# Optimization experiments

Measured on AMD Instinct MI355X. Metric: run time of the kernel, lower is better.

Reference implementation:

```python
import jax, jax.numpy as jnp
import numpy as np

B, LX, LY, D = 8, 2048, 2048, 256

def setup_inputs() -> dict:
    key = jax.random.key(0)
    k1, k2, k3, k4 = jax.random.split(key, 4)
    x = jax.random.normal(k1, (B, LX, D), dtype=jnp.float32)
    y = jax.random.normal(k2, (B, LY, D), dtype=jnp.float32)
    y_mask = jax.random.randint(k3, (B, LY), 0, 2).astype(jnp.bool_)
    W = jax.random.normal(k4, (D, D), dtype=jnp.float32) * (1.0 / np.sqrt(D))
    b = jnp.zeros((D,), dtype=jnp.float32)
    return {"x": x, "y": y, "y_mask": y_mask, "W": W, "b": b}

def reference(x, y, y_mask, W, b):
    # shared linear + relu projection (torch Linear: x @ W.T + b)
    x_proj = jax.nn.relu(jnp.einsum('bld,ed->ble', x, W) + b)  # [B,LX,D]
    y_proj = jax.nn.relu(jnp.einsum('bld,ed->ble', y, W) + b)  # [B,LY,D]
    scores = jnp.einsum('bxd,byd->bxy', x_proj, y_proj)        # [B,LX,LY]
    scores = jnp.where(y_mask[:, None, :], -jnp.inf, scores)
    alpha = jax.nn.softmax(scores, axis=-1)                    # [B,LX,LY]
    return jnp.einsum('bxy,byd->bxd', alpha, y)                # [B,LX,D]
```

## Files before the change

### kernel.cpp

```cpp
#include <hip/hip_runtime.h>

typedef __attribute__((ext_vector_type(8))) short short8;
typedef _Float16 half8 __attribute__((ext_vector_type(8)));
typedef __attribute__((ext_vector_type(4))) float f32x4;
typedef __attribute__((ext_vector_type(4))) unsigned int uint4v;
typedef __attribute__((ext_vector_type(2))) unsigned int uint2v;

#define B_   8
#define LX_  2048
#define LY_  2048
#define D_   256
#define NROW (B_ * LX_)

__device__ __forceinline__ unsigned short f2bf(float f) {
  unsigned u = __builtin_bit_cast(unsigned, f);
  u += 0x7FFF + ((u >> 16) & 1);
  return (unsigned short)(u >> 16);
}
__device__ __forceinline__ float bf2f(unsigned short h) {
  unsigned u = ((unsigned)h) << 16;
  return __builtin_bit_cast(float, u);
}

__global__ __launch_bounds__(256) void wsplit_kernel(
    const float* __restrict__ W, unsigned short* __restrict__ Whi,
    unsigned short* __restrict__ Wlo) {
  int i = blockIdx.x * 256 + threadIdx.x;
  float w = W[i];
  unsigned short hi = f2bf(w);
  Whi[i] = hi;
  Wlo[i] = f2bf(w - bf2f(hi));
}

__global__ __launch_bounds__(256) void scan_kernel(
    const int* __restrict__ MASK, int* __restrict__ CIDX,
    int* __restrict__ CPOS, int* __restrict__ Lc) {
  __shared__ int s[256];
  int b = blockIdx.x, t = threadIdx.x;
  int f[8];
  int cnt = 0;
  for (int k = 0; k < 8; ++k) {
    f[k] = (MASK[b * 2048 + t * 8 + k] == 0) ? 1 : 0;
    cnt += f[k];
  }
  s[t] = cnt;
  __syncthreads();
  for (int off = 1; off < 256; off <<= 1) {
    int v = (t >= off) ? s[t - off] : 0;
    __syncthreads();
    s[t] += v;
    __syncthreads();
  }
  if (t == 255) Lc[b] = s[255];
  int off = s[t] - cnt;
  for (int k = 0; k < 8; ++k) {
    int j = t * 8 + k;
    if (f[k]) {
      CIDX[b * 2048 + off] = j;
      CPOS[b * 2048 + j] = b * 2048 + off;
      ++off;
    } else {
      CPOS[b * 2048 + j] = -1;
    }
  }
}

__global__ __launch_bounds__(256) void zero_tail_kernel(
    const int* __restrict__ Lc, _Float16* __restrict__ YPc) {
  int b = blockIdx.x;
  int lc = Lc[b];
  int end = (lc + 31) & ~31;
  int total = (end - lc) * 32;
  for (int c = threadIdx.x; c < total; c += 256) {
    int rr = c >> 5, seg = c & 31;
    uint4v z = {0, 0, 0, 0};
    *(uint4v*)(YPc + (size_t)(b * 2048 + lc + rr) * D_ + seg * 8) = z;
  }
}

__global__ __launch_bounds__(256, 2) void proj_kernel(
    const float* __restrict__ X, const float* __restrict__ Y,
    const float* __restrict__ bias,
    const unsigned short* __restrict__ Whi, const unsigned short* __restrict__ Wlo,
    const int* __restrict__ CPOS,
    _Float16* __restrict__ XP, _Float16* __restrict__ YPc) {
  __shared__ unsigned short Ah[64][40], Al[64][40];
  __shared__ unsigned short Bh[256][40], Bl[256][40];

  int t = threadIdx.x;
  int lane = t & 63, wave = t >> 6;
  int q = lane >> 4, n15 = lane & 15;

  bool isX = blockIdx.x < 256;
  const float* src = isX ? X : Y;
  int m0 = (isX ? blockIdx.x : (blockIdx.x - 256)) * 64;

  f32x4 acc[4][4];
  for (int mt = 0; mt < 4; ++mt)
    for (int nt = 0; nt < 4; ++nt) acc[mt][nt] = (f32x4){0.f, 0.f, 0.f, 0.f};

  int arow = t >> 2, aseg = t & 3;
  int erow = t >> 2, ec = t & 3;

  f32x4 pa[2];
  uint4v pbh[4], pbl[4];
#define PROJ_PF(kc)                                                            \
  {                                                                            \
    for (int i = 0; i < 2; ++i)                                                \
      pa[i] = *(const f32x4*)(src + (size_t)(m0 + arow) * D_ + (kc) * 32 +     \
                              (aseg + i * 4) * 4);                             \
    for (int p = 0; p < 4; ++p) {                                              \
      int e = p * 64 + erow;                                                   \
      pbh[p] = *(const uint4v*)(Whi + (size_t)e * D_ + (kc) * 32 + ec * 8);    \
      pbl[p] = *(const uint4v*)(Wlo + (size_t)e * D_ + (kc) * 32 + ec * 8);    \
    }                                                                          \
  }

  PROJ_PF(0);

  for (int kc = 0; kc < 8; ++kc) {
    __syncthreads();
    for (int i = 0; i < 2; ++i) {
      int seg = aseg + i * 4;
      f32x4 f = pa[i];
      unsigned short h[4], l[4];
      for (int j = 0; j < 4; ++j) {
        h[j] = f2bf(f[j]);
        l[j] = f2bf(f[j] - bf2f(h[j]));
      }
      uint2v vh = {(unsigned)h[0] | ((unsigned)h[1] << 16),
                   (unsigned)h[2] | ((unsigned)h[3] << 16)};
      uint2v vl = {(unsigned)l[0] | ((unsigned)l[1] << 16),
                   (unsigned)l[2] | ((unsigned)l[3] << 16)};
      *(uint2v*)&Ah[arow][seg * 4] = vh;
      *(uint2v*)&Al[arow][seg * 4] = vl;
    }
    for (int p = 0; p < 4; ++p) {
      int e = p * 64 + erow;
      *(uint4v*)&Bh[e][ec * 8] = pbh[p];
      *(uint4v*)&Bl[e][ec * 8] = pbl[p];
    }
    if (kc < 7) PROJ_PF(kc + 1);
    __syncthreads();

    short8 afh[4], afl[4], bfh[4], bfl[4];
    for (int mt = 0; mt < 4; ++mt) {
      afh[mt] = *(const short8*)&Ah[mt * 16 + n15][q * 8];
      afl[mt] = *(const short8*)&Al[mt * 16 + n15][q * 8];
    }
    for (int nt = 0; nt < 4; ++nt) {
      bfh[nt] = *(const short8*)&Bh[wave * 64 + nt * 16 + n15][q * 8];
      bfl[nt] = *(const short8*)&Bl[wave * 64 + nt * 16 + n15][q * 8];
    }
    for (int mt = 0; mt < 4; ++mt)
      for (int nt = 0; nt < 4; ++nt) {
        acc[mt][nt] = __builtin_amdgcn_mfma_f32_16x16x32_bf16(afh[mt], bfh[nt], acc[mt][nt], 0, 0, 0);
        acc[mt][nt] = __builtin_amdgcn_mfma_f32_16x16x32_bf16(afl[mt], bfh[nt], acc[mt][nt], 0, 0, 0);
        acc[mt][nt] = __builtin_amdgcn_mfma_f32_16x16x32_bf16(afh[mt], bfl[nt], acc[mt][nt], 0, 0, 0);
      }
  }
#undef PROJ_PF

  int drow[16];
  for (int mt = 0; mt < 4; ++mt)
    for (int r = 0; r < 4; ++r) {
      int row = m0 + mt * 16 + q * 4 + r;
      drow[mt * 4 + r] = isX ? row : CPOS[row];
    }
  _Float16* dst = isX ? XP : YPc;
  for (int nt = 0; nt < 4; ++nt) {
    int e = wave * 64 + nt * 16 + n15;
    float bv = bias[e];
    for (int mt = 0; mt < 4; ++mt)
      for (int r = 0; r < 4; ++r) {
        int dr = drow[mt * 4 + r];
        if (dr >= 0) {
          float v = acc[mt][nt][r] + bv;
          v = v > 0.f ? v : 0.f;
          dst[(size_t)dr * D_ + e] = (_Float16)v;
        }
      }
  }
}

__global__ __launch_bounds__(256) void gatherT_kernel(
    const float* __restrict__ Y, const int* __restrict__ CIDX,
    const int* __restrict__ Lc, _Float16* __restrict__ YTc) {
  __shared__ _Float16 tile[64][72];
  int id = blockIdx.x;
  int db = id & 3, nb = (id >> 2) & 31, b = id >> 7;
  int lc = Lc[b];
  int end = (lc + 31) & ~31;
  if (nb * 64 >= end) return;
  int t = threadIdx.x;
  int nl = t >> 2, ds = t & 3;
  int j = nb * 64 + nl;
  int idx = (j < lc) ? CIDX[b * 2048 + j] : 0;
  const float* src = Y + (size_t)(b * LY_ + idx) * D_ + db * 64 + ds * 16;
  for (int i = 0; i < 4; ++i) {
    f32x4 f = *(const f32x4*)(src + i * 4);
    for (int k = 0; k < 4; ++k) tile[ds * 16 + i * 4 + k][nl] = (_Float16)f[k];
  }
  __syncthreads();
  int dl = t >> 2, nsub = t & 3;
  uint4v v0 = *(const uint4v*)&tile[dl][nsub * 16];
  uint4v v1 = *(const uint4v*)&tile[dl][nsub * 16 + 8];
  _Float16* dst = YTc + (size_t)(b * D_ + db * 64 + dl) * LY_ + nb * 64 + nsub * 16;
  *(uint4v*)(dst) = v0;
  *(uint4v*)(dst + 8) = v1;
}

__global__ __launch_bounds__(256, 2) void flash_kernel(
    const _Float16* __restrict__ XP, const _Float16* __restrict__ YPc,
    const _Float16* __restrict__ YTc, const int* __restrict__ Lc,
    _Float16* __restrict__ PO, float* __restrict__ Pm, float* __restrict__ Pl) {
  __shared__ _Float16 yp_t[32][264];
  __shared__ _Float16 yT_t[256][40];
  __shared__ _Float16 pbuf[4][16][40];

  int t = threadIdx.x;
  int lane = t & 63, wave = t >> 6;
  int q = lane >> 4, n15 = lane & 15;
  int half = blockIdx.x & 1;
  int xb = (blockIdx.x >> 1) & 31;
  int b = blockIdx.x >> 6;
  int row0 = xb * 64 + wave * 16;

  int lc = Lc[b];
  int T  = (lc + 31) >> 5;
  int T0 = (T + 1) >> 1;
  int tstart = half ? T0 : 0;
  int tend   = half ? T  : T0;

  half8 a[8];
  const _Float16* xrow = XP + (size_t)(b * LX_ + row0 + n15) * D_ + q * 8;
  for (int kk = 0; kk < 8; ++kk) a[kk] = *(const half8*)(xrow + kk * 32);

  half8 lones;
  for (int j = 0; j < 8; ++j) lones[j] = (n15 == 0) ? (_Float16)1 : (_Float16)0;

  float m_r[4];
  for (int r = 0; r < 4; ++r) m_r[r] = -1e30f;
  f32x4 lacc = {0.f, 0.f, 0.f, 0.f};
  f32x4 oacc[16];
  for (int dt = 0; dt < 16; ++dt) oacc[dt] = (f32x4){0.f, 0.f, 0.f, 0.f};

  const _Float16* ypb = YPc + (size_t)b * LY_ * D_;
  const _Float16* yTb = YTc + (size_t)b * D_ * LY_;

  uint4v pr[8];
#define PREFETCH(tt)                                                          \
  {                                                                           \
    int y0p = (tt) * 32;                                                      \
    for (int i = 0; i < 4; ++i) {                                             \
      int c = t + i * 256;                                                    \
      pr[i] = *(const uint4v*)(ypb + (size_t)(y0p + (c >> 5)) * D_ + (c & 31) * 8); \
    }                                                                         \
    for (int i = 0; i < 4; ++i) {                                             \
      int c = t + i * 256;                                                    \
      pr[4 + i] = *(const uint4v*)(yTb + (size_t)(c >> 2) * LY_ + y0p + (c & 3) * 8); \
    }                                                                         \
  }

  if (tstart < tend) PREFETCH(tstart);

  for (int tt = tstart; tt < tend; ++tt) {
    int y0 = tt * 32;
    __syncthreads();
    for (int i = 0; i < 4; ++i) {
      int c = t + i * 256;
      *(uint4v*)&yp_t[c >> 5][(c & 31) * 8] = pr[i];
    }
    for (int i = 0; i < 4; ++i) {
      int c = t + i * 256;
      *(uint4v*)&yT_t[c >> 2][(c & 3) * 8] = pr[4 + i];
    }
    if (tt + 1 < tend) PREFETCH(tt + 1);
    __syncthreads();

    f32x4 S0 = {0.f, 0.f, 0.f, 0.f}, S1 = {0.f, 0.f, 0.f, 0.f};
    for (int kk = 0; kk < 8; ++kk) {
      half8 b0 = *(const half8*)&yp_t[n15][kk * 32 + q * 8];
      S0 = __builtin_amdgcn_mfma_f32_16x16x32_f16(a[kk], b0, S0, 0, 0, 0);
    }
    for (int kk = 0; kk < 8; ++kk) {
      half8 b1 = *(const half8*)&yp_t[16 + n15][kk * 32 + q * 8];
      S1 = __builtin_amdgcn_mfma_f32_16x16x32_f16(a[kk], b1, S1, 0, 0, 0);
    }
    bool mk0 = (y0 + n15) >= lc;
    bool mk1 = (y0 + 16 + n15) >= lc;

    float al[4];
    _Float16 ph0[4], ph1[4];
    bool need = false;
    for (int r = 0; r < 4; ++r) {
      float s0 = mk0 ? -1e30f : S0[r];
      float s1 = mk1 ? -1e30f : S1[r];
      float tm = fmaxf(s0, s1);
      tm = fmaxf(tm, __shfl_xor(tm, 1));
      tm = fmaxf(tm, __shfl_xor(tm, 2));
      tm = fmaxf(tm, __shfl_xor(tm, 4));
      tm = fmaxf(tm, __shfl_xor(tm, 8));
      float mn = fmaxf(m_r[r], tm);
      al[r] = __expf(m_r[r] - mn);
      m_r[r] = mn;
      ph0[r] = (_Float16)__expf(s0 - mn);
      ph1[r] = (_Float16)__expf(s1 - mn);
      need = need || (al[r] != 1.0f);
    }
    if (__ballot(need)) {
      for (int dt = 0; dt < 16; ++dt)
        for (int r = 0; r < 4; ++r) oacc[dt][r] *= al[r];
      for (int r = 0; r < 4; ++r) lacc[r] *= al[r];
    }
    for (int r = 0; r < 4; ++r) {
      pbuf[wave][q * 4 + r][n15] = ph0[r];
      pbuf[wave][q * 4 + r][16 + n15] = ph1[r];
    }
    half8 pa = *(const half8*)&pbuf[wave][n15][q * 8];
    lacc = __builtin_amdgcn_mfma_f32_16x16x32_f16(pa, lones, lacc, 0, 0, 0);
    for (int dt = 0; dt < 16; ++dt) {
      half8 bb = *(const half8*)&yT_t[dt * 16 + n15][q * 8];
      oacc[dt] = __builtin_amdgcn_mfma_f32_16x16x32_f16(pa, bb, oacc[dt], 0, 0, 0);
    }
  }
#undef PREFETCH

  size_t prow = (size_t)(half * B_ + b) * LX_ + row0;
  _Float16* po = PO + prow * D_;
  for (int dt = 0; dt < 16; ++dt)
    for (int r = 0; r < 4; ++r)
      po[(size_t)(q * 4 + r) * D_ + dt * 16 + n15] = (_Float16)oacc[dt][r];
  if (n15 == 0) {
    for (int r = 0; r < 4; ++r) {
      Pm[prow + q * 4 + r] = m_r[r];
      Pl[prow + q * 4 + r] = lacc[r];
    }
  }
}

__global__ __launch_bounds__(256) void merge_kernel(
    const _Float16* __restrict__ PO, const float* __restrict__ Pm,
    const float* __restrict__ Pl, float* __restrict__ OUT) {
  int c = blockIdx.x * 256 + threadIdx.x;
  int row = c >> 5, seg = c & 31;
  float m0 = Pm[row], m1 = Pm[NROW + row];
  float l0 = Pl[row], l1 = Pl[NROW + row];
  float m = fmaxf(m0, m1);
  float w0 = __expf(m0 - m), w1 = __expf(m1 - m);
  float inv = 1.0f / (l0 * w0 + l1 * w1);
  const _Float16* p0 = PO + (size_t)row * D_ + seg * 8;
  const _Float16* p1 = p0 + (size_t)NROW * D_;
  half8 a = *(const half8*)p0;
  half8 bsec = *(const half8*)p1;
  float* o = OUT + (size_t)row * D_ + seg * 8;
  f32x4 o0, o1;
  for (int j = 0; j < 4; ++j) o0[j] = ((float)a[j] * w0 + (float)bsec[j] * w1) * inv;
  for (int j = 0; j < 4; ++j) o1[j] = ((float)a[4 + j] * w0 + (float)bsec[4 + j] * w1) * inv;
  *(f32x4*)o = o0;
  *(f32x4*)(o + 4) = o1;
}

extern "C" void kernel_launch(void* const* d_in, const int* in_sizes, int n_in,
                              void* d_out, int out_size, void* d_ws, size_t ws_size,
                              hipStream_t stream) {
  const float* x     = (const float*)d_in[0];
  const float* y     = (const float*)d_in[1];
  const int*   ymask = (const int*)  d_in[2];
  const float* W     = (const float*)d_in[3];
  const float* bias  = (const float*)d_in[4];
  float* out = (float*)d_out;

  char* ws = (char*)d_ws;
  unsigned short* Whi = (unsigned short*)(ws);
  unsigned short* Wlo = (unsigned short*)(ws + 131072);
  _Float16* XP  = (_Float16*)(ws + 262144);
  _Float16* YPc = (_Float16*)(ws + 262144 + 8388608);
  _Float16* YTc = (_Float16*)(ws + 262144 + 2 * 8388608);
  _Float16* PO  = (_Float16*)(ws + 262144 + 3 * 8388608);
  char* tail = ws + 262144 + 3 * 8388608 + 16777216;
  float* Pm   = (float*)(tail);
  float* Pl   = (float*)(tail + 131072);
  int*   CIDX = (int*)  (tail + 262144);
  int*   CPOS = (int*)  (tail + 262144 + 65536);
  int*   Lc   = (int*)  (tail + 262144 + 131072);

  wsplit_kernel<<<256, 256, 0, stream>>>(W, Whi, Wlo);
  scan_kernel<<<8, 256, 0, stream>>>(ymask, CIDX, CPOS, Lc);
  zero_tail_kernel<<<8, 256, 0, stream>>>(Lc, YPc);
  proj_kernel<<<512, 256, 0, stream>>>(x, y, bias, Whi, Wlo, CPOS, XP, YPc);
  gatherT_kernel<<<1024, 256, 0, stream>>>(y, CIDX, Lc, YTc);
  flash_kernel<<<512, 256, 0, stream>>>(XP, YPc, YTc, Lc, PO, Pm, Pl);
  merge_kernel<<<2048, 256, 0, stream>>>(PO, Pm, Pl, out);
}
```

Before: 166.6 us.

## Pre-split X/Y into bf16 hi/lo planes and merge setup kernels

Adds a separate pass that converts X and Y into bf16 hi/lo planes in the workspace, so the projection GEMM loads ready bf16 tiles instead of converting fp32 in its inner loop. The W split and the mask scan are merged into one launch with vectorized W conversion. The tail-zeroing kernel for the compacted Y projection is removed, and the PO buffer now shares memory with the split planes. The extra pass adds a full read and write of the inputs in exchange for less ALU work inside the GEMM, and dropping the tail zeroing relies on the flash kernel not reading those padding rows.

Result: slower. 172.1 us (+3.3%).

```diff
diff --git a/kernel.cpp b/kernel.cpp
--- a/kernel.cpp
+++ b/kernel.cpp
@@ -11,6 +11,7 @@
 #define LY_  2048
 #define D_   256
 #define NROW (B_ * LX_)
+#define MTOT (2 * NROW)
 
 __device__ __forceinline__ unsigned short f2bf(float f) {
   unsigned u = __builtin_bit_cast(unsigned, f);
@@ -22,21 +23,32 @@
   return __builtin_bit_cast(float, u);
 }
 
-__global__ __launch_bounds__(256) void wsplit_kernel(
+__global__ __launch_bounds__(256) void prep_kernel(
     const float* __restrict__ W, unsigned short* __restrict__ Whi,
-    unsigned short* __restrict__ Wlo) {
-  int i = blockIdx.x * 256 + threadIdx.x;
-  float w = W[i];
-  unsigned short hi = f2bf(w);
-  Whi[i] = hi;
-  Wlo[i] = f2bf(w - bf2f(hi));
-}
-
-__global__ __launch_bounds__(256) void scan_kernel(
+    unsigned short* __restrict__ Wlo,
     const int* __restrict__ MASK, int* __restrict__ CIDX,
     int* __restrict__ CPOS, int* __restrict__ Lc) {
+  int t = threadIdx.x;
+  if (blockIdx.x >= 8) {
+    int base = (blockIdx.x - 8) * 2048 + t * 8;
+    f32x4 f0 = *(const f32x4*)(W + base);
+    f32x4 f1 = *(const f32x4*)(W + base + 4);
+    float v[8] = {f0[0], f0[1], f0[2], f0[3], f1[0], f1[1], f1[2], f1[3]};
+    unsigned short h[8], l[8];
+    for (int j = 0; j < 8; ++j) {
+      h[j] = f2bf(v[j]);
+      l[j] = f2bf(v[j] - bf2f(h[j]));
+    }
+    uint4v vh = {(unsigned)h[0] | ((unsigned)h[1] << 16), (unsigned)h[2] | ((unsigned)h[3] << 16),
+                 (unsigned)h[4] | ((unsigned)h[5] << 16), (unsigned)h[6] | ((unsigned)h[7] << 16)};
+    uint4v vl = {(unsigned)l[0] | ((unsigned)l[1] << 16), (unsigned)l[2] | ((unsigned)l[3] << 16),
+                 (unsigned)l[4] | ((unsigned)l[5] << 16), (unsigned)l[6] | ((unsigned)l[7] << 16)};
+    *(uint4v*)(Whi + base) = vh;
+    *(uint4v*)(Wlo + base) = vl;
+    return;
+  }
   __shared__ int s[256];
-  int b = blockIdx.x, t = threadIdx.x;
+  int b = blockIdx.x;
   int f[8];
   int cnt = 0;
   for (int k = 0; k < 8; ++k) {
@@ -65,21 +77,33 @@
   }
 }
 
-__global__ __launch_bounds__(256) void zero_tail_kernel(
-    const int* __restrict__ Lc, _Float16* __restrict__ YPc) {
-  int b = blockIdx.x;
-  int lc = Lc[b];
-  int end = (lc + 31) & ~31;
-  int total = (end - lc) * 32;
-  for (int c = threadIdx.x; c < total; c += 256) {
-    int rr = c >> 5, seg = c & 31;
-    uint4v z = {0, 0, 0, 0};
-    *(uint4v*)(YPc + (size_t)(b * 2048 + lc + rr) * D_ + seg * 8) = z;
-  }
+__global__ __launch_bounds__(256) void split_xy_kernel(
+    const float* __restrict__ X, const float* __restrict__ Y,
+    unsigned short* __restrict__ XYhi, unsigned short* __restrict__ XYlo) {
+  int bb = blockIdx.x;
+  const float* src;
+  size_t off;
+  if (bb < 2048) { src = X; off = 0; }
+  else           { src = Y; off = (size_t)NROW * D_; bb -= 2048; }
+  size_t e0 = ((size_t)bb * 256 + threadIdx.x) * 8;
+  f32x4 f0 = *(const f32x4*)(src + e0);
+  f32x4 f1 = *(const f32x4*)(src + e0 + 4);
+  float v[8] = {f0[0], f0[1], f0[2], f0[3], f1[0], f1[1], f1[2], f1[3]};
+  unsigned short h[8], l[8];
+  for (int j = 0; j < 8; ++j) {
+    h[j] = f2bf(v[j]);
+    l[j] = f2bf(v[j] - bf2f(h[j]));
+  }
+  uint4v vh = {(unsigned)h[0] | ((unsigned)h[1] << 16), (unsigned)h[2] | ((unsigned)h[3] << 16),
+               (unsigned)h[4] | ((unsigned)h[5] << 16), (unsigned)h[6] | ((unsigned)h[7] << 16)};
+  uint4v vl = {(unsigned)l[0] | ((unsigned)l[1] << 16), (unsigned)l[2] | ((unsigned)l[3] << 16),
+               (unsigned)l[4] | ((unsigned)l[5] << 16), (unsigned)l[6] | ((unsigned)l[7] << 16)};
+  *(uint4v*)(XYhi + off + e0) = vh;
+  *(uint4v*)(XYlo + off + e0) = vl;
 }
 
 __global__ __launch_bounds__(256, 2) void proj_kernel(
-    const float* __restrict__ X, const float* __restrict__ Y,
+    const unsigned short* __restrict__ XYhi, const unsigned short* __restrict__ XYlo,
     const float* __restrict__ bias,
     const unsigned short* __restrict__ Whi, const unsigned short* __restrict__ Wlo,
     const int* __restrict__ CPOS,
@@ -92,8 +116,7 @@
   int q = lane >> 4, n15 = lane & 15;
 
   bool isX = blockIdx.x < 256;
-  const float* src = isX ? X : Y;
-  int m0 = (isX ? blockIdx.x : (blockIdx.x - 256)) * 64;
+  int m0 = blockIdx.x * 64;
 
   f32x4 acc[4][4];
   for (int mt = 0; mt < 4; ++mt)
@@ -102,13 +125,12 @@
   int arow = t >> 2, aseg = t & 3;
   int erow = t >> 2, ec = t & 3;
 
-  f32x4 pa[2];
-  uint4v pbh[4], pbl[4];
+  uint4v pah, pal, pbh[4], pbl[4];
 #define PROJ_PF(kc)                                                            \
   {                                                                            \
-    for (int i = 0; i < 2; ++i)                                                \
-      pa[i] = *(const f32x4*)(src + (size_t)(m0 + arow) * D_ + (kc) * 32 +     \
-                              (aseg + i * 4) * 4);                             \
+    size_t aoff = (size_t)(m0 + arow) * D_ + (kc) * 32 + aseg * 8;             \
+    pah = *(const uint4v*)(XYhi + aoff);                                       \
+    pal = *(const uint4v*)(XYlo + aoff);                                       \
     for (int p = 0; p < 4; ++p) {                                              \
       int e = p * 64 + erow;                                                   \
       pbh[p] = *(const uint4v*)(Whi + (size_t)e * D_ + (kc) * 32 + ec * 8);    \
@@ -120,21 +142,8 @@
 
   for (int kc = 0; kc < 8; ++kc) {
     __syncthreads();
-    for (int i = 0; i < 2; ++i) {
-      int seg = aseg + i * 4;
-      f32x4 f = pa[i];
-      unsigned short h[4], l[4];
-      for (int j = 0; j < 4; ++j) {
-        h[j] = f2bf(f[j]);
-        l[j] = f2bf(f[j] - bf2f(h[j]));
-      }
-      uint2v vh = {(unsigned)h[0] | ((unsigned)h[1] << 16),
-                   (unsigned)h[2] | ((unsigned)h[3] << 16)};
-      uint2v vl = {(unsigned)l[0] | ((unsigned)l[1] << 16),
-                   (unsigned)l[2] | ((unsigned)l[3] << 16)};
-      *(uint2v*)&Ah[arow][seg * 4] = vh;
-      *(uint2v*)&Al[arow][seg * 4] = vl;
-    }
+    *(uint4v*)&Ah[arow][aseg * 8] = pah;
+    *(uint4v*)&Al[arow][aseg * 8] = pal;
     for (int p = 0; p < 4; ++p) {
       int e = p * 64 + erow;
       *(uint4v*)&Bh[e][ec * 8] = pbh[p];
@@ -165,7 +174,7 @@
   for (int mt = 0; mt < 4; ++mt)
     for (int r = 0; r < 4; ++r) {
       int row = m0 + mt * 16 + q * 4 + r;
-      drow[mt * 4 + r] = isX ? row : CPOS[row];
+      drow[mt * 4 + r] = isX ? row : CPOS[row - NROW];
     }
   _Float16* dst = isX ? XP : YPc;
   for (int nt = 0; nt < 4; ++nt) {
@@ -372,23 +381,24 @@
   float* out = (float*)d_out;
 
   char* ws = (char*)d_ws;
-  unsigned short* Whi = (unsigned short*)(ws);
-  unsigned short* Wlo = (unsigned short*)(ws + 131072);
-  _Float16* XP  = (_Float16*)(ws + 262144);
-  _Float16* YPc = (_Float16*)(ws + 262144 + 8388608);
-  _Float16* YTc = (_Float16*)(ws + 262144 + 2 * 8388608);
-  _Float16* PO  = (_Float16*)(ws + 262144 + 3 * 8388608);
-  char* tail = ws + 262144 + 3 * 8388608 + 16777216;
-  float* Pm   = (float*)(tail);
-  float* Pl   = (float*)(tail + 131072);
-  int*   CIDX = (int*)  (tail + 262144);
-  int*   CPOS = (int*)  (tail + 262144 + 65536);
-  int*   Lc   = (int*)  (tail + 262144 + 131072);
-
-  wsplit_kernel<<<256, 256, 0, stream>>>(W, Whi, Wlo);
-  scan_kernel<<<8, 256, 0, stream>>>(ymask, CIDX, CPOS, Lc);
-  zero_tail_kernel<<<8, 256, 0, stream>>>(Lc, YPc);
-  proj_kernel<<<512, 256, 0, stream>>>(x, y, bias, Whi, Wlo, CPOS, XP, YPc);
+  size_t o = 0;
+  unsigned short* Whi  = (unsigned short*)(ws + o); o += 131072;
+  unsigned short* Wlo  = (unsigned short*)(ws + o); o += 131072;
+  unsigned short* XYhi = (unsigned short*)(ws + o);
+  _Float16*       PO   = (_Float16*)(ws + o);       o += (size_t)MTOT * D_ * 2;
+  unsigned short* XYlo = (unsigned short*)(ws + o); o += (size_t)MTOT * D_ * 2;
+  _Float16* XP  = (_Float16*)(ws + o); o += 8388608;
+  _Float16* YPc = (_Float16*)(ws + o); o += 8388608;
+  _Float16* YTc = (_Float16*)(ws + o); o += 8388608;
+  float* Pm   = (float*)(ws + o); o += 131072;
+  float* Pl   = (float*)(ws + o); o += 131072;
+  int*   CIDX = (int*)  (ws + o); o += 65536;
+  int*   CPOS = (int*)  (ws + o); o += 65536;
+  int*   Lc   = (int*)  (ws + o);
+
+  prep_kernel<<<40, 256, 0, stream>>>(W, Whi, Wlo, ymask, CIDX, CPOS, Lc);
+  split_xy_kernel<<<4096, 256, 0, stream>>>(x, y, XYhi, XYlo);
+  proj_kernel<<<512, 256, 0, stream>>>(XYhi, XYlo, bias, Whi, Wlo, CPOS, XP, YPc);
   gatherT_kernel<<<1024, 256, 0, stream>>>(y, CIDX, Lc, YTc);
   flash_kernel<<<512, 256, 0, stream>>>(XP, YPc, YTc, Lc, PO, Pm, Pl);
   merge_kernel<<<2048, 256, 0, stream>>>(PO, Pm, Pl, out);
```

## Split flash attention four ways over keys and fuse prep and projection launches

Applied to the files above, without the earlier changes.

The flash kernel now splits the compacted key range into four parts instead of two, which doubles the grid to 1024 blocks. The merge kernel combines four partial softmax results. The weight split and mask scan are fused into one prep kernel, and the projection and transposed gather are fused into one launch. The zero-tail kernel is removed. This cuts launch count and adds parallelism, but doubles the partial-output traffic written and read by merge, and repeats the per-block query load and output store.

Result: no change. 165.5 us (-0.7%).

```diff
diff --git a/kernel.cpp b/kernel.cpp
--- a/kernel.cpp
+++ b/kernel.cpp
@@ -11,6 +11,7 @@
 #define LY_  2048
 #define D_   256
 #define NROW (B_ * LX_)
+#define NQ   4
 
 __device__ __forceinline__ unsigned short f2bf(float f) {
   unsigned u = __builtin_bit_cast(unsigned, f);
@@ -22,21 +23,32 @@
   return __builtin_bit_cast(float, u);
 }
 
-__global__ __launch_bounds__(256) void wsplit_kernel(
+__global__ __launch_bounds__(256) void prep_kernel(
     const float* __restrict__ W, unsigned short* __restrict__ Whi,
-    unsigned short* __restrict__ Wlo) {
-  int i = blockIdx.x * 256 + threadIdx.x;
-  float w = W[i];
-  unsigned short hi = f2bf(w);
-  Whi[i] = hi;
-  Wlo[i] = f2bf(w - bf2f(hi));
-}
-
-__global__ __launch_bounds__(256) void scan_kernel(
+    unsigned short* __restrict__ Wlo,
     const int* __restrict__ MASK, int* __restrict__ CIDX,
     int* __restrict__ CPOS, int* __restrict__ Lc) {
+  int t = threadIdx.x;
+  if (blockIdx.x >= 8) {
+    int base = (blockIdx.x - 8) * 2048 + t * 8;
+    f32x4 f0 = *(const f32x4*)(W + base);
+    f32x4 f1 = *(const f32x4*)(W + base + 4);
+    float v[8] = {f0[0], f0[1], f0[2], f0[3], f1[0], f1[1], f1[2], f1[3]};
+    unsigned short h[8], l[8];
+    for (int j = 0; j < 8; ++j) {
+      h[j] = f2bf(v[j]);
+      l[j] = f2bf(v[j] - bf2f(h[j]));
+    }
+    uint4v vh = {(unsigned)h[0] | ((unsigned)h[1] << 16), (unsigned)h[2] | ((unsigned)h[3] << 16),
+                 (unsigned)h[4] | ((unsigned)h[5] << 16), (unsigned)h[6] | ((unsigned)h[7] << 16)};
+    uint4v vl = {(unsigned)l[0] | ((unsigned)l[1] << 16), (unsigned)l[2] | ((unsigned)l[3] << 16),
+                 (unsigned)l[4] | ((unsigned)l[5] << 16), (unsigned)l[6] | ((unsigned)l[7] << 16)};
+    *(uint4v*)(Whi + base) = vh;
+    *(uint4v*)(Wlo + base) = vl;
+    return;
+  }
   __shared__ int s[256];
-  int b = blockIdx.x, t = threadIdx.x;
+  int b = blockIdx.x;
   int f[8];
   int cnt = 0;
   for (int k = 0; k < 8; ++k) {
@@ -65,29 +77,47 @@
   }
 }
 
-__global__ __launch_bounds__(256) void zero_tail_kernel(
-    const int* __restrict__ Lc, _Float16* __restrict__ YPc) {
-  int b = blockIdx.x;
-  int lc = Lc[b];
-  int end = (lc + 31) & ~31;
-  int total = (end - lc) * 32;
-  for (int c = threadIdx.x; c < total; c += 256) {
-    int rr = c >> 5, seg = c & 31;
-    uint4v z = {0, 0, 0, 0};
-    *(uint4v*)(YPc + (size_t)(b * 2048 + lc + rr) * D_ + seg * 8) = z;
-  }
-}
-
-__global__ __launch_bounds__(256, 2) void proj_kernel(
+__global__ __launch_bounds__(256, 2) void projgather_kernel(
     const float* __restrict__ X, const float* __restrict__ Y,
     const float* __restrict__ bias,
     const unsigned short* __restrict__ Whi, const unsigned short* __restrict__ Wlo,
-    const int* __restrict__ CPOS,
-    _Float16* __restrict__ XP, _Float16* __restrict__ YPc) {
-  __shared__ unsigned short Ah[64][40], Al[64][40];
-  __shared__ unsigned short Bh[256][40], Bl[256][40];
-
+    const int* __restrict__ CPOS, const int* __restrict__ CIDX,
+    const int* __restrict__ Lc,
+    _Float16* __restrict__ XP, _Float16* __restrict__ YPc,
+    _Float16* __restrict__ YTc) {
+  __shared__ __align__(16) unsigned char smem[51200];
   int t = threadIdx.x;
+
+  if (blockIdx.x >= 512) {
+    _Float16 (*tile)[72] = (_Float16(*)[72])smem;
+    int id = blockIdx.x - 512;
+    int db = id & 3, nb = (id >> 2) & 31, b = id >> 7;
+    int lc = Lc[b];
+    int end = (lc + 31) & ~31;
+    if (nb * 64 >= end) return;
+    int nl = t >> 2, ds = t & 3;
+    int j = nb * 64 + nl;
+    int idx = (j < lc) ? CIDX[b * 2048 + j] : 0;
+    const float* src = Y + (size_t)(b * LY_ + idx) * D_ + db * 64 + ds * 16;
+    for (int i = 0; i < 4; ++i) {
+      f32x4 f = *(const f32x4*)(src + i * 4);
+      for (int k = 0; k < 4; ++k) tile[ds * 16 + i * 4 + k][nl] = (_Float16)f[k];
+    }
+    __syncthreads();
+    int dl = t >> 2, nsub = t & 3;
+    uint4v v0 = *(const uint4v*)&tile[dl][nsub * 16];
+    uint4v v1 = *(const uint4v*)&tile[dl][nsub * 16 + 8];
+    _Float16* dst = YTc + (size_t)(b * D_ + db * 64 + dl) * LY_ + nb * 64 + nsub * 16;
+    *(uint4v*)(dst) = v0;
+    *(uint4v*)(dst + 8) = v1;
+    return;
+  }
+
+  unsigned short (*Ah)[40] = (unsigned short(*)[40])(smem);
+  unsigned short (*Al)[40] = (unsigned short(*)[40])(smem + 5120);
+  unsigned short (*Bh)[40] = (unsigned short(*)[40])(smem + 10240);
+  unsigned short (*Bl)[40] = (unsigned short(*)[40])(smem + 30720);
+
   int lane = t & 63, wave = t >> 6;
   int q = lane >> 4, n15 = lane & 15;
 
@@ -183,33 +213,6 @@
   }
 }
 
-__global__ __launch_bounds__(256) void gatherT_kernel(
-    const float* __restrict__ Y, const int* __restrict__ CIDX,
-    const int* __restrict__ Lc, _Float16* __restrict__ YTc) {
-  __shared__ _Float16 tile[64][72];
-  int id = blockIdx.x;
-  int db = id & 3, nb = (id >> 2) & 31, b = id >> 7;
-  int lc = Lc[b];
-  int end = (lc + 31) & ~31;
-  if (nb * 64 >= end) return;
-  int t = threadIdx.x;
-  int nl = t >> 2, ds = t & 3;
-  int j = nb * 64 + nl;
-  int idx = (j < lc) ? CIDX[b * 2048 + j] : 0;
-  const float* src = Y + (size_t)(b * LY_ + idx) * D_ + db * 64 + ds * 16;
-  for (int i = 0; i < 4; ++i) {
-    f32x4 f = *(const f32x4*)(src + i * 4);
-    for (int k = 0; k < 4; ++k) tile[ds * 16 + i * 4 + k][nl] = (_Float16)f[k];
-  }
-  __syncthreads();
-  int dl = t >> 2, nsub = t & 3;
-  uint4v v0 = *(const uint4v*)&tile[dl][nsub * 16];
-  uint4v v1 = *(const uint4v*)&tile[dl][nsub * 16 + 8];
-  _Float16* dst = YTc + (size_t)(b * D_ + db * 64 + dl) * LY_ + nb * 64 + nsub * 16;
-  *(uint4v*)(dst) = v0;
-  *(uint4v*)(dst + 8) = v1;
-}
-
 __global__ __launch_bounds__(256, 2) void flash_kernel(
     const _Float16* __restrict__ XP, const _Float16* __restrict__ YPc,
     const _Float16* __restrict__ YTc, const int* __restrict__ Lc,
@@ -221,16 +224,15 @@
   int t = threadIdx.x;
   int lane = t & 63, wave = t >> 6;
   int q = lane >> 4, n15 = lane & 15;
-  int half = blockIdx.x & 1;
-  int xb = (blockIdx.x >> 1) & 31;
-  int b = blockIdx.x >> 6;
+  int qtr = blockIdx.x & 3;
+  int xb = (blockIdx.x >> 2) & 31;
+  int b = blockIdx.x >> 7;
   int row0 = xb * 64 + wave * 16;
 
   int lc = Lc[b];
-  int T  = (lc + 31) >> 5;
-  int T0 = (T + 1) >> 1;
-  int tstart = half ? T0 : 0;
-  int tend   = half ? T  : T0;
+  int T = (lc + 31) >> 5;
+  int tstart = (T * qtr) >> 2;
+  int tend   = (T * (qtr + 1)) >> 2;
 
   half8 a[8];
   const _Float16* xrow = XP + (size_t)(b * LX_ + row0 + n15) * D_ + q * 8;
@@ -326,7 +328,7 @@
   }
 #undef PREFETCH
 
-  size_t prow = (size_t)(half * B_ + b) * LX_ + row0;
+  size_t prow = (size_t)(qtr * B_ + b) * LX_ + row0;
   _Float16* po = PO + prow * D_;
   for (int dt = 0; dt < 16; ++dt)
     for (int r = 0; r < 4; ++r)
@@ -344,21 +346,32 @@
     const float* __restrict__ Pl, float* __restrict__ OUT) {
   int c = blockIdx.x * 256 + threadIdx.x;
   int row = c >> 5, seg = c & 31;
-  float m0 = Pm[row], m1 = Pm[NROW + row];
-  float l0 = Pl[row], l1 = Pl[NROW + row];
-  float m = fmaxf(m0, m1);
-  float w0 = __expf(m0 - m), w1 = __expf(m1 - m);
-  float inv = 1.0f / (l0 * w0 + l1 * w1);
-  const _Float16* p0 = PO + (size_t)row * D_ + seg * 8;
-  const _Float16* p1 = p0 + (size_t)NROW * D_;
-  half8 a = *(const half8*)p0;
-  half8 bsec = *(const half8*)p1;
-  float* o = OUT + (size_t)row * D_ + seg * 8;
-  f32x4 o0, o1;
-  for (int j = 0; j < 4; ++j) o0[j] = ((float)a[j] * w0 + (float)bsec[j] * w1) * inv;
-  for (int j = 0; j < 4; ++j) o1[j] = ((float)a[4 + j] * w0 + (float)bsec[4 + j] * w1) * inv;
-  *(f32x4*)o = o0;
-  *(f32x4*)(o + 4) = o1;
+  float m = -1e30f;
+  float mh[NQ], lh[NQ];
+  for (int h = 0; h < NQ; ++h) {
+    mh[h] = Pm[(size_t)h * NROW + row];
+    lh[h] = Pl[(size_t)h * NROW + row];
+    m = fmaxf(m, mh[h]);
+  }
+  float l = 0.f;
+  float wh[NQ];
+  for (int h = 0; h < NQ; ++h) {
+    wh[h] = __expf(mh[h] - m);
+    l += lh[h] * wh[h];
+  }
+  float inv = 1.0f / l;
+  float o[8];
+  for (int j = 0; j < 8; ++j) o[j] = 0.f;
+  for (int h = 0; h < NQ; ++h) {
+    half8 a = *(const half8*)(PO + ((size_t)h * NROW + row) * D_ + seg * 8);
+    float w = wh[h];
+    for (int j = 0; j < 8; ++j) o[j] += (float)a[j] * w;
+  }
+  float* op = OUT + (size_t)row * D_ + seg * 8;
+  f32x4 o0 = {o[0] * inv, o[1] * inv, o[2] * inv, o[3] * inv};
+  f32x4 o1 = {o[4] * inv, o[5] * inv, o[6] * inv, o[7] * inv};
+  *(f32x4*)op = o0;
+  *(f32x4*)(op + 4) = o1;
 }
 
 extern "C" void kernel_launch(void* const* d_in, const int* in_sizes, int n_in,
@@ -372,24 +385,22 @@
   float* out = (float*)d_out;
 
   char* ws = (char*)d_ws;
-  unsigned short* Whi = (unsigned short*)(ws);
-  unsigned short* Wlo = (unsigned short*)(ws + 131072);
-  _Float16* XP  = (_Float16*)(ws + 262144);
-  _Float16* YPc = (_Float16*)(ws + 262144 + 8388608);
-  _Float16* YTc = (_Float16*)(ws + 262144 + 2 * 8388608);
-  _Float16* PO  = (_Float16*)(ws + 262144 + 3 * 8388608);
-  char* tail = ws + 262144 + 3 * 8388608 + 16777216;
-  float* Pm   = (float*)(tail);
-  float* Pl   = (float*)(tail + 131072);
-  int*   CIDX = (int*)  (tail + 262144);
-  int*   CPOS = (int*)  (tail + 262144 + 65536);
-  int*   Lc   = (int*)  (tail + 262144 + 131072);
-
-  wsplit_kernel<<<256, 256, 0, stream>>>(W, Whi, Wlo);
-  scan_kernel<<<8, 256, 0, stream>>>(ymask, CIDX, CPOS, Lc);
-  zero_tail_kernel<<<8, 256, 0, stream>>>(Lc, YPc);
-  proj_kernel<<<512, 256, 0, stream>>>(x, y, bias, Whi, Wlo, CPOS, XP, YPc);
-  gatherT_kernel<<<1024, 256, 0, stream>>>(y, CIDX, Lc, YTc);
-  flash_kernel<<<512, 256, 0, stream>>>(XP, YPc, YTc, Lc, PO, Pm, Pl);
+  size_t o = 0;
+  unsigned short* Whi = (unsigned short*)(ws + o); o += 131072;
+  unsigned short* Wlo = (unsigned short*)(ws + o); o += 131072;
+  _Float16* XP  = (_Float16*)(ws + o); o += 8388608;
+  _Float16* YPc = (_Float16*)(ws + o); o += 8388608;
+  _Float16* YTc = (_Float16*)(ws + o); o += 8388608;
+  _Float16* PO  = (_Float16*)(ws + o); o += (size_t)NQ * NROW * D_ * 2;
+  float* Pm   = (float*)(ws + o); o += (size_t)NQ * NROW * 4;
+  float* Pl   = (float*)(ws + o); o += (size_t)NQ * NROW * 4;
+  int*   CIDX = (int*)  (ws + o); o += 65536;
+  int*   CPOS = (int*)  (ws + o); o += 65536;
+  int*   Lc   = (int*)  (ws + o);
+
+  prep_kernel<<<40, 256, 0, stream>>>(W, Whi, Wlo, ymask, CIDX, CPOS, Lc);
+  projgather_kernel<<<1536, 256, 0, stream>>>(x, y, bias, Whi, Wlo, CPOS, CIDX, Lc,
+                                              XP, YPc, YTc);
+  flash_kernel<<<1024, 256, 0, stream>>>(XP, YPc, YTc, Lc, PO, Pm, Pl);
   merge_kernel<<<2048, 256, 0, stream>>>(PO, Pm, Pl, out);
 }
```
